# Kernel optimization log

Measured on AMD Instinct MI355X. Metric: run time of the kernel, lower is better.

Reference implementation:

```python
import jax, jax.numpy as jnp
import numpy as np

B, S, E = 4, 2048, 1024

def setup_inputs() -> dict:
    key = jax.random.key(0)
    ks = jax.random.split(key, 9)
    lim = 1.0 / np.sqrt(E)
    inp = {
        "query": jax.random.normal(ks[0], (B, S, E), dtype=jnp.float32),
        "key": jax.random.normal(ks[1], (B, S, E), dtype=jnp.float32),
        "value": jax.random.normal(ks[2], (B, S, E), dtype=jnp.float32),
        "Wq": jax.random.uniform(ks[3], (E, E), jnp.float32, -lim, lim),
        "bq": jax.random.uniform(ks[4], (E,), jnp.float32, -lim, lim),
        "Wk": jax.random.uniform(ks[5], (E, E), jnp.float32, -lim, lim),
        "bk": jax.random.uniform(ks[6], (E,), jnp.float32, -lim, lim),
        "Wv": jax.random.uniform(ks[7], (E, E), jnp.float32, -lim, lim),
        "bv": jax.random.uniform(ks[8], (E,), jnp.float32, -lim, lim),
    }
    return inp

def reference(query, key, value, Wq, bq, Wk, bk, Wv, bv):
    # Linear layers (torch stores weight as [out,in]; here W is [in,out] used as x @ W)
    q = query @ Wq + bq            # [B,S,E]
    k = key @ Wk + bk              # [B,S,E]
    v = value @ Wv + bv            # [B,S,E]
    inv_scale = jnp.asarray(E, q.dtype) ** 0.5
    scores = jnp.einsum("bse,bte->bst", q, k) / inv_scale  # [B,S,S]
    attn = jax.nn.softmax(scores, axis=-1)
    # dropout_p = 0.0 -> identity
    out = jnp.einsum("bst,bte->bse", attn, v)  # [B,S,E]
    return out
```

## Files before the change

kernel.cpp:

```cpp
#include <hip/hip_runtime.h>
#include <hip/hip_bf16.h>


typedef __bf16 bf16_t;
typedef bf16_t bf16x8 __attribute__((ext_vector_type(8)));
typedef bf16_t bf16x4 __attribute__((ext_vector_type(4)));
typedef float  f32x4  __attribute__((ext_vector_type(4)));

typedef const __attribute__((address_space(1))) unsigned gl_uint;
typedef __attribute__((address_space(3))) unsigned lds_uint;

#define BM 128
#define BN 128
#define BK 64

__device__ __forceinline__ void gload_lds16(const void* g, void* l) {
  __builtin_amdgcn_global_load_lds((gl_uint*)g, (lds_uint*)l, 16, 0, 0);
}

#define VMCNT(N) asm volatile("s_waitcnt vmcnt(" #N ")" ::: "memory")
#define LGKM0()  asm volatile("s_waitcnt lgkmcnt(0)" ::: "memory")

template <int KS, int NT>
__device__ __forceinline__ void gemm_v3(
    const bf16_t* __restrict__ Ab, const bf16_t* __restrict__ Bb,
    bf16_t* Lb, f32x4 acc[4][4])
{
  const int tid  = threadIdx.x;
  const int lane = tid & 63;
  const int l15  = lane & 15;
  const int quad = lane >> 4;
  const int wid  = tid >> 6;
  const int wr   = wid >> 1;
  const int wcl  = wid & 1;
  const int swz0 = (quad ^ (l15 & 7)) * 8;
  const int swz1 = ((quad + 4) ^ (l15 & 7)) * 8;

  const int r8 = tid >> 3, s8 = tid & 7;
  const size_t gbase = (size_t)r8 * KS + (size_t)((s8 ^ (r8 & 7)) * 8);
  const int dbase = tid * 8;

#define SLOTA(s) (Lb + (s) * 24576)
#define SLOTB(s) (Lb + (s) * 24576 + 16384)
#define STAGE6(ktile, slot) { \
    const bf16_t* _A = Ab + (size_t)(ktile) * 64; \
    const bf16_t* _B = Bb + (size_t)(ktile) * 64; \
    bf16_t* _la = SLOTA(slot); bf16_t* _lb = SLOTB(slot); \
    gload_lds16(_A + gbase,                      _la + dbase); \
    gload_lds16(_A + gbase + (size_t)64 * KS,    _la + dbase + 4096); \
    gload_lds16(_A + gbase + (size_t)128 * KS,   _la + dbase + 8192); \
    gload_lds16(_A + gbase + (size_t)192 * KS,   _la + dbase + 12288); \
    gload_lds16(_B + gbase,                      _lb + dbase); \
    gload_lds16(_B + gbase + (size_t)64 * KS,    _lb + dbase + 4096); }

  const int aoff = (wr * 64 + l15) * 64;
  const int boff = (wcl * 64 + l15) * 64;

#define RD(slot, FA, FB) { \
    const bf16_t* _a = SLOTA(slot) + aoff; \
    const bf16_t* _b = SLOTB(slot) + boff; \
    _Pragma("unroll") for (int mi = 0; mi < 4; ++mi) { \
      FA[mi][0] = *(const bf16x8*)(_a + mi * 1024 + swz0); \
      FA[mi][1] = *(const bf16x8*)(_a + mi * 1024 + swz1); } \
    _Pragma("unroll") for (int ni = 0; ni < 4; ++ni) { \
      FB[ni][0] = *(const bf16x8*)(_b + ni * 1024 + swz0); \
      FB[ni][1] = *(const bf16x8*)(_b + ni * 1024 + swz1); } }

#define MFM(FA, FB) \
    _Pragma("unroll") for (int kk = 0; kk < 2; ++kk) \
    _Pragma("unroll") for (int mi = 0; mi < 4; ++mi) \
    _Pragma("unroll") for (int ni = 0; ni < 4; ++ni) \
      acc[mi][ni] = __builtin_amdgcn_mfma_f32_16x16x32_bf16( \
          FA[mi][kk], FB[ni][kk], acc[mi][ni], 0, 0, 0);

  bf16x8 fa0[4][2], fb0[4][2], fa1[4][2], fb1[4][2];

  STAGE6(0, 0); STAGE6(1, 1); STAGE6(2, 2);
  VMCNT(6);
  __builtin_amdgcn_s_barrier();
  RD(0, fa0, fb0);
  LGKM0();
  __builtin_amdgcn_s_barrier();

#pragma unroll
  for (int kt = 0; kt < NT - 2; ++kt) {
    const int ss = kt % 3;
    const int rs = (kt + 1) % 3;
    if (kt <= NT - 4) STAGE6(kt + 3, ss);
    if ((kt & 1) == 0) { RD(rs, fa1, fb1); MFM(fa0, fb0); }
    else               { RD(rs, fa0, fb0); MFM(fa1, fb1); }
    if (kt <= NT - 4) { VMCNT(6); }
    else              { VMCNT(0); }
    __builtin_amdgcn_s_barrier();
  }
  RD((NT - 1) % 3, fa1, fb1); MFM(fa0, fb0);
  MFM(fa1, fb1);

#undef SLOTA
#undef SLOTB
#undef STAGE6
#undef RD
#undef MFM
}

__device__ __forceinline__ void mfma_tile128(const bf16_t* As, const bf16_t* Bs,
                                             f32x4 acc[4][4]) {
  const int lane = threadIdx.x & 63;
  const int quad = lane >> 4;
  const int l15  = lane & 15;
  const int wid  = threadIdx.x >> 6;
  const int wm   = (wid >> 1) * 64;
  const int wn   = (wid & 1) * 64;
  const int csw  = l15 & 7;
#pragma unroll
  for (int ks = 0; ks < 2; ++ks) {
    const int sg = ks * 4 + quad;
    const int c  = (sg ^ csw) * 8;
    bf16x8 fa[4], fb[4];
#pragma unroll
    for (int i = 0; i < 4; ++i)
      fa[i] = *(const bf16x8*)&As[(wm + i * 16 + l15) * BK + c];
#pragma unroll
    for (int i = 0; i < 4; ++i)
      fb[i] = *(const bf16x8*)&Bs[(wn + i * 16 + l15) * BK + c];
#pragma unroll
    for (int mi = 0; mi < 4; ++mi)
#pragma unroll
      for (int ni = 0; ni < 4; ++ni)
        acc[mi][ni] = __builtin_amdgcn_mfma_f32_16x16x32_bf16(
            fa[mi], fb[ni], acc[mi][ni], 0, 0, 0);
  }
}

__device__ __forceinline__ void gemm_core128(
    const bf16_t* __restrict__ Ab, const bf16_t* __restrict__ Bb,
    const int K, bf16_t* As, bf16_t* Bs, f32x4 acc[4][4])
{
  const int tid = threadIdx.x;
  for (int kt = 0; kt < K; kt += BK) {
#pragma unroll
    for (int j = 0; j < 4; ++j) {
      const int lin = j * 256 + tid;
      const int row = lin >> 3;
      const int seg = (lin & 7) ^ (row & 7);
      gload_lds16(Ab + (size_t)row * K + kt + seg * 8, &As[lin * 8]);
    }
#pragma unroll
    for (int j = 0; j < 4; ++j) {
      const int lin = j * 256 + tid;
      const int row = lin >> 3;
      const int seg = (lin & 7) ^ (row & 7);
      gload_lds16(Bb + (size_t)row * K + kt + seg * 8, &Bs[lin * 8]);
    }
    __syncthreads();
    mfma_tile128(As, Bs, acc);
    __syncthreads();
  }
}

__global__ __launch_bounds__(256, 2)
void qkv_proj(const bf16_t* __restrict__ qb, const bf16_t* __restrict__ kb,
              const bf16_t* __restrict__ vb, const bf16_t* __restrict__ Wqt,
              const bf16_t* __restrict__ Wkt, const bf16_t* __restrict__ Wvt,
              const float* __restrict__ bq, const float* __restrict__ bk,
              const float* __restrict__ bv, bf16_t* __restrict__ qp,
              bf16_t* __restrict__ kp, bf16_t* __restrict__ vT)
{
  __shared__ __align__(16) bf16_t As[BM * BK];
  __shared__ __align__(16) bf16_t Bs[BN * BK];

  const int L = blockIdx.x;
  const int g = L >> 3;
  const int gst = (L & 7) * 3 + (g >> 6);
  const int z  = gst >> 3;
  const int sy = gst & 7;
  const int w  = g & 63;
  const int bx = w & 7;
  const int by = sy * 8 + (w >> 3);

  const bf16_t* A    = (z == 0) ? qb : (z == 1) ? kb : vb;
  const bf16_t* W    = (z == 0) ? Wqt : (z == 1) ? Wkt : Wvt;
  const float*  bias = (z == 0) ? bq : (z == 1) ? bk : bv;
  const int K = 1024, N = 1024;
  const bf16_t* Ab = A + (size_t)by * BM * K;
  const bf16_t* Bb = W + (size_t)bx * BN * K;

  f32x4 acc[4][4];
  const f32x4 z4 = {0.f, 0.f, 0.f, 0.f};
#pragma unroll
  for (int i = 0; i < 4; ++i)
#pragma unroll
    for (int j = 0; j < 4; ++j) acc[i][j] = z4;

  gemm_core128(Ab, Bb, K, As, Bs, acc);

  const int lane = threadIdx.x & 63;
  const int quad = lane >> 4;
  const int l15  = lane & 15;
  const int wid  = threadIdx.x >> 6;
  const int wm = (wid >> 1) * 64, wn = (wid & 1) * 64;
  const int m0 = by * BM, n0 = bx * BN;
#pragma unroll
  for (int mi = 0; mi < 4; ++mi) {
#pragma unroll
    for (int ni = 0; ni < 4; ++ni) {
      const int gn = n0 + wn + ni * 16 + l15;
      const int gm = m0 + wm + mi * 16 + quad * 4;
      const float bv_ = bias[gn];
      f32x4 a = acc[mi][ni];
      if (z < 2) {
        bf16_t* C = (z == 0) ? qp : kp;
#pragma unroll
        for (int r = 0; r < 4; ++r)
          C[(size_t)(gm + r) * N + gn] = (bf16_t)(a[r] + bv_);
      } else {
        const int b = gm >> 11;
        const int s = gm & 2047;
        bf16x4 o;
#pragma unroll
        for (int r = 0; r < 4; ++r) o[r] = (bf16_t)(a[r] + bv_);
        *(bf16x4*)&vT[((size_t)b * N + gn) * 2048 + s] = o;
      }
    }
  }
}

__global__ __launch_bounds__(512, 2)
void scores_v3(const bf16_t* __restrict__ qp, const bf16_t* __restrict__ kp,
               bf16_t* __restrict__ P, float* __restrict__ lsum)
{
  __shared__ __align__(16) bf16_t lds[3 * 24576];
  const int L   = blockIdx.x;
  const int lin = (L & 7) * 64 + (L >> 3);
  const int bz  = lin >> 7;
  const int r   = lin & 127;
  const int by  = r >> 4, bx = r & 15;
  const int K = 1024;

  const bf16_t* Ab = qp + (size_t)bz * 2048 * 1024 + (size_t)by * 256 * K;
  const bf16_t* Bb = kp + (size_t)bz * 2048 * 1024 + (size_t)bx * 128 * K;

  f32x4 acc[4][4];
  const f32x4 z4 = {0.f, 0.f, 0.f, 0.f};
#pragma unroll
  for (int i = 0; i < 4; ++i)
#pragma unroll
    for (int j = 0; j < 4; ++j) acc[i][j] = z4;

  gemm_v3<1024, 16>(Ab, Bb, lds, acc);

  const int tid = threadIdx.x;
  const int lane = tid & 63, l15 = lane & 15, quad = lane >> 4;
  const int wid = tid >> 6, wr = wid >> 1, wcl = wid & 1;
  const int m0 = by * 256 + wr * 64;
  const int n0 = bx * 128 + wcl * 64;
  bf16_t* C = P + (size_t)bz * 2048 * 2048;
  float* lsb = lsum + (size_t)bz * 2048;
  const float cexp = 0.03125f * 1.4426950408889634f;
#pragma unroll
  for (int mi = 0; mi < 4; ++mi) {
    const int gm = m0 + mi * 16 + quad * 4;
#pragma unroll
    for (int rr = 0; rr < 4; ++rr) {
      float rs = 0.f;
#pragma unroll
      for (int ni = 0; ni < 4; ++ni) {
        const int gn = n0 + ni * 16 + l15;
        const bf16_t ob = (bf16_t)exp2f(acc[mi][ni][rr] * cexp);
        C[(size_t)(gm + rr) * 2048 + gn] = ob;
        rs += (float)ob;
      }
      rs += __shfl_xor(rs, 1, 64);
      rs += __shfl_xor(rs, 2, 64);
      rs += __shfl_xor(rs, 4, 64);
      rs += __shfl_xor(rs, 8, 64);
      if (l15 == 0) atomicAdd(&lsb[gm + rr], rs);
    }
  }
}

__global__ __launch_bounds__(256, 2)
void pv128(const bf16_t* __restrict__ P, const bf16_t* __restrict__ vT,
           const float* __restrict__ lsum, float* __restrict__ out)
{
  __shared__ __align__(16) bf16_t As[BM * BK];
  __shared__ __align__(16) bf16_t Bs[BN * BK];

  const int L = blockIdx.x;
  const int xcd = L & 7;
  const int w = (L >> 3) & 63;
  const int bz = xcd >> 1;
  const int bx = w & 7;
  const int by = (xcd & 1) * 8 + (w >> 3);

  const bf16_t* Ab = P  + (size_t)bz * 2048 * 2048 + (size_t)by * BM * 2048;
  const bf16_t* Bb = vT + (size_t)bz * 1024 * 2048 + (size_t)bx * BN * 2048;

  f32x4 acc[4][4];
  const f32x4 z4 = {0.f, 0.f, 0.f, 0.f};
#pragma unroll
  for (int i = 0; i < 4; ++i)
#pragma unroll
    for (int j = 0; j < 4; ++j) acc[i][j] = z4;

  gemm_core128(Ab, Bb, 2048, As, Bs, acc);

  const int lane = threadIdx.x & 63;
  const int quad = lane >> 4;
  const int l15  = lane & 15;
  const int wid  = threadIdx.x >> 6;
  const int wm = (wid >> 1) * 64, wn = (wid & 1) * 64;
  const int m0 = by * BM, n0 = bx * BN;
  const float* ls = lsum + (size_t)bz * 2048;
  float* C = out + (size_t)bz * 2048 * 1024;
#pragma unroll
  for (int mi = 0; mi < 4; ++mi) {
    const int gm = m0 + wm + mi * 16 + quad * 4;
    const f32x4 lv = *(const f32x4*)&ls[gm];
    float il[4];
#pragma unroll
    for (int r = 0; r < 4; ++r) il[r] = 1.0f / lv[r];
#pragma unroll
    for (int ni = 0; ni < 4; ++ni) {
      const int gn = n0 + wn + ni * 16 + l15;
      f32x4 a = acc[mi][ni];
#pragma unroll
      for (int r = 0; r < 4; ++r)
        C[(size_t)(gm + r) * 1024 + gn] = a[r] * il[r];
    }
  }
}

__global__ __launch_bounds__(256)
void prep(const float* __restrict__ q, const float* __restrict__ k,
          const float* __restrict__ v, const float* __restrict__ Wq,
          const float* __restrict__ Wk, const float* __restrict__ Wv,
          bf16_t* __restrict__ qo, bf16_t* __restrict__ ko,
          bf16_t* __restrict__ vo, bf16_t* __restrict__ Wqt,
          bf16_t* __restrict__ Wkt, bf16_t* __restrict__ Wvt) {
  const int L = blockIdx.x;
  const int tid = threadIdx.x;
  if (L < 24576) {
    const int z = L >> 13;
    const int blk = L & 8191;
    const float* in = (z == 0) ? q : (z == 1) ? k : v;
    bf16_t* out = (z == 0) ? qo : (z == 1) ? ko : vo;
    const size_t i = ((size_t)blk * 256 + tid) * 4;
    const float4 w = *(const float4*)(in + i);
    bf16x4 o;
    o[0] = (bf16_t)w.x; o[1] = (bf16_t)w.y; o[2] = (bf16_t)w.z; o[3] = (bf16_t)w.w;
    *(bf16x4*)(out + i) = o;
  } else {
    const int t = L - 24576;
    const int z = t >> 8;
    const int wi = t & 255;
    const float* W = (z == 0) ? Wq : (z == 1) ? Wk : Wv;
    bf16_t* Wt = (z == 0) ? Wqt : (z == 1) ? Wkt : Wvt;
    __shared__ float tile[64][65];
    const int n0 = (wi & 15) * 64;
    const int k0 = (wi >> 4) * 64;
#pragma unroll
    for (int it = 0; it < 16; ++it) {
      const int idx = it * 256 + tid;
      const int r = idx >> 6, c = idx & 63;
      tile[r][c] = W[(size_t)(k0 + r) * 1024 + n0 + c];
    }
    __syncthreads();
#pragma unroll
    for (int it = 0; it < 16; ++it) {
      const int idx = it * 256 + tid;
      const int r = idx >> 6, c = idx & 63;
      Wt[(size_t)(n0 + r) * 1024 + k0 + c] = (bf16_t)tile[c][r];
    }
  }
}

extern "C" void kernel_launch(void* const* d_in, const int* in_sizes, int n_in,
                              void* d_out, int out_size, void* d_ws, size_t ws_size,
                              hipStream_t stream) {
  const int B = 4, S = 2048, E = 1024;
  const size_t BSE = (size_t)B * S * E;
  const size_t EE  = (size_t)E * E;

  const float* q_in = (const float*)d_in[0];
  const float* k_in = (const float*)d_in[1];
  const float* v_in = (const float*)d_in[2];
  const float* Wq = (const float*)d_in[3];
  const float* bq = (const float*)d_in[4];
  const float* Wk = (const float*)d_in[5];
  const float* bk = (const float*)d_in[6];
  const float* Wv = (const float*)d_in[7];
  const float* bv = (const float*)d_in[8];
  float* out = (float*)d_out;

  char* ws = (char*)d_ws;
  bf16_t* Wqt = (bf16_t*)ws;
  bf16_t* Wkt = Wqt + EE;
  bf16_t* Wvt = Wkt + EE;
  bf16_t* qb  = Wvt + EE;
  bf16_t* kb  = qb + BSE;
  bf16_t* vb  = kb + BSE;
  bf16_t* qp  = vb + BSE;
  bf16_t* kp  = qp + BSE;
  bf16_t* vT  = kp + BSE;
  bf16_t* P   = vT + BSE;
  float* lsum = (float*)qb;

  prep<<<25344, 256, 0, stream>>>(q_in, k_in, v_in, Wq, Wk, Wv,
                                  qb, kb, vb, Wqt, Wkt, Wvt);

  qkv_proj<<<1536, 256, 0, stream>>>(qb, kb, vb, Wqt, Wkt, Wvt,
                                     bq, bk, bv, qp, kp, vT);

  hipMemsetAsync(lsum, 0, (size_t)B * S * sizeof(float), stream);

  scores_v3<<<512, 512, 0, stream>>>(qp, kp, P, lsum);

  pv128<<<512, 256, 0, stream>>>(P, vT, lsum, out);

  (void)in_sizes; (void)n_in; (void)out_size; (void)ws_size;
}
```

Before: 302.0 us.

## Fuse fp32-to-bf16 input cast into QKV GEMM and compute softmax row sums via MFMA

The separate prep pass that cast q/k/v activations to bf16 is removed. The QKV projection kernel now loads fp32 activations into registers, converts them and writes bf16 into LDS, double-buffering the register loads across k-tiles. The softmax denominator is no longer built with shuffles and atomics in the scores kernel. It is instead accumulated in the PV GEMM by an extra MFMA of each P fragment against a vector of ones. This drops the memset, the atomics and an extra read and write of the activations. In exchange it adds a few MFMAs per k-step and uses register-path A loads instead of direct-to-LDS loads.

```diff
diff --git a/kernel.cpp b/kernel.cpp
--- a/kernel.cpp
+++ b/kernel.cpp
@@ -20,6 +20,190 @@
 
 #define VMCNT(N) asm volatile("s_waitcnt vmcnt(" #N ")" ::: "memory")
 #define LGKM0()  asm volatile("s_waitcnt lgkmcnt(0)" ::: "memory")
+
+template <bool LSUM>
+__device__ __forceinline__ void mfma_tile128(const bf16_t* As, const bf16_t* Bs,
+                                             f32x4 acc[4][4], f32x4 acc_l[4]) {
+  const int lane = threadIdx.x & 63;
+  const int quad = lane >> 4;
+  const int l15  = lane & 15;
+  const int wid  = threadIdx.x >> 6;
+  const int wm   = (wid >> 1) * 64;
+  const int wn   = (wid & 1) * 64;
+  const int csw  = l15 & 7;
+  bf16x8 ones;
+  if (LSUM) {
+#pragma unroll
+    for (int t = 0; t < 8; ++t) ones[t] = (bf16_t)1.0f;
+  }
+#pragma unroll
+  for (int ks = 0; ks < 2; ++ks) {
+    const int sg = ks * 4 + quad;
+    const int c  = (sg ^ csw) * 8;
+    bf16x8 fa[4], fb[4];
+#pragma unroll
+    for (int i = 0; i < 4; ++i)
+      fa[i] = *(const bf16x8*)&As[(wm + i * 16 + l15) * BK + c];
+#pragma unroll
+    for (int i = 0; i < 4; ++i)
+      fb[i] = *(const bf16x8*)&Bs[(wn + i * 16 + l15) * BK + c];
+#pragma unroll
+    for (int mi = 0; mi < 4; ++mi)
+#pragma unroll
+      for (int ni = 0; ni < 4; ++ni)
+        acc[mi][ni] = __builtin_amdgcn_mfma_f32_16x16x32_bf16(
+            fa[mi], fb[ni], acc[mi][ni], 0, 0, 0);
+    if (LSUM) {
+#pragma unroll
+      for (int mi = 0; mi < 4; ++mi)
+        acc_l[mi] = __builtin_amdgcn_mfma_f32_16x16x32_bf16(
+            fa[mi], ones, acc_l[mi], 0, 0, 0);
+    }
+  }
+}
+
+template <bool LSUM>
+__device__ __forceinline__ void gemm_core128(
+    const bf16_t* __restrict__ Ab, const bf16_t* __restrict__ Bb,
+    const int K, bf16_t* As, bf16_t* Bs, f32x4 acc[4][4], f32x4 acc_l[4])
+{
+  const int tid = threadIdx.x;
+  for (int kt = 0; kt < K; kt += BK) {
+#pragma unroll
+    for (int j = 0; j < 4; ++j) {
+      const int lin = j * 256 + tid;
+      const int row = lin >> 3;
+      const int seg = (lin & 7) ^ (row & 7);
+      gload_lds16(Ab + (size_t)row * K + kt + seg * 8, &As[lin * 8]);
+    }
+#pragma unroll
+    for (int j = 0; j < 4; ++j) {
+      const int lin = j * 256 + tid;
+      const int row = lin >> 3;
+      const int seg = (lin & 7) ^ (row & 7);
+      gload_lds16(Bb + (size_t)row * K + kt + seg * 8, &Bs[lin * 8]);
+    }
+    __syncthreads();
+    mfma_tile128<LSUM>(As, Bs, acc, acc_l);
+    __syncthreads();
+  }
+}
+
+__global__ __launch_bounds__(256, 2)
+void qkv_f(const float* __restrict__ qin, const float* __restrict__ kin,
+           const float* __restrict__ vin, const bf16_t* __restrict__ Wqt,
+           const bf16_t* __restrict__ Wkt, const bf16_t* __restrict__ Wvt,
+           const float* __restrict__ bq, const float* __restrict__ bk,
+           const float* __restrict__ bv, bf16_t* __restrict__ qp,
+           bf16_t* __restrict__ kp, bf16_t* __restrict__ vT)
+{
+  __shared__ __align__(16) bf16_t As[BM * BK];
+  __shared__ __align__(16) bf16_t Bs[BN * BK];
+
+  const int L = blockIdx.x;
+  const int g = L >> 3;
+  const int gst = (L & 7) * 3 + (g >> 6);
+  const int z  = gst >> 3;
+  const int sy = gst & 7;
+  const int w  = g & 63;
+  const int bx = w & 7;
+  const int by = sy * 8 + (w >> 3);
+
+  const float*  A    = (z == 0) ? qin : (z == 1) ? kin : vin;
+  const bf16_t* W    = (z == 0) ? Wqt : (z == 1) ? Wkt : Wvt;
+  const float*  bias = (z == 0) ? bq : (z == 1) ? bk : bv;
+  const int K = 1024, N = 1024;
+  const float*  Ab = A + (size_t)by * BM * K;
+  const bf16_t* Bb = W + (size_t)bx * BN * K;
+
+  const int tid = threadIdx.x;
+
+  f32x4 acc[4][4];
+  const f32x4 z4 = {0.f, 0.f, 0.f, 0.f};
+#pragma unroll
+  for (int i = 0; i < 4; ++i)
+#pragma unroll
+    for (int j = 0; j < 4; ++j) acc[i][j] = z4;
+
+#define LOAD_A(ktile, AR) { \
+    _Pragma("unroll") for (int j = 0; j < 4; ++j) { \
+      const int lin = j * 256 + tid; \
+      const int row = lin >> 3; \
+      const int seg = (lin & 7) ^ (row & 7); \
+      const float* _s = Ab + (size_t)row * K + (ktile) * 64 + seg * 8; \
+      AR[2 * j]     = *(const float4*)_s; \
+      AR[2 * j + 1] = *(const float4*)(_s + 4); } }
+
+#define WRITE_A(AR) { \
+    _Pragma("unroll") for (int j = 0; j < 4; ++j) { \
+      const int lin = j * 256 + tid; \
+      bf16x8 o; \
+      o[0] = (bf16_t)AR[2 * j].x;     o[1] = (bf16_t)AR[2 * j].y; \
+      o[2] = (bf16_t)AR[2 * j].z;     o[3] = (bf16_t)AR[2 * j].w; \
+      o[4] = (bf16_t)AR[2 * j + 1].x; o[5] = (bf16_t)AR[2 * j + 1].y; \
+      o[6] = (bf16_t)AR[2 * j + 1].z; o[7] = (bf16_t)AR[2 * j + 1].w; \
+      *(bf16x8*)&As[lin * 8] = o; } }
+
+  float4 ar0[8], ar1[8];
+  LOAD_A(0, ar0);
+
+#pragma unroll
+  for (int t16 = 0; t16 < 16; ++t16) {
+    const int kt = t16 * 64;
+#pragma unroll
+    for (int j = 0; j < 4; ++j) {
+      const int lin = j * 256 + tid;
+      const int row = lin >> 3;
+      const int seg = (lin & 7) ^ (row & 7);
+      gload_lds16(Bb + (size_t)row * K + kt + seg * 8, &Bs[lin * 8]);
+    }
+    __builtin_amdgcn_sched_barrier(0);
+    if (t16 < 15) {
+      if ((t16 & 1) == 0) { LOAD_A(t16 + 1, ar1); }
+      else                { LOAD_A(t16 + 1, ar0); }
+    }
+    if ((t16 & 1) == 0) { WRITE_A(ar0); }
+    else                { WRITE_A(ar1); }
+    if (t16 < 15) { VMCNT(8); }
+    else          { VMCNT(0); }
+    LGKM0();
+    __builtin_amdgcn_s_barrier();
+    mfma_tile128<false>(As, Bs, acc, nullptr);
+    __builtin_amdgcn_s_barrier();
+  }
+#undef LOAD_A
+#undef WRITE_A
+
+  const int lane = tid & 63;
+  const int quad = lane >> 4;
+  const int l15  = lane & 15;
+  const int wid  = tid >> 6;
+  const int wm = (wid >> 1) * 64, wn = (wid & 1) * 64;
+  const int m0 = by * BM, n0 = bx * BN;
+#pragma unroll
+  for (int mi = 0; mi < 4; ++mi) {
+#pragma unroll
+    for (int ni = 0; ni < 4; ++ni) {
+      const int gn = n0 + wn + ni * 16 + l15;
+      const int gm = m0 + wm + mi * 16 + quad * 4;
+      const float bv_ = bias[gn];
+      f32x4 a = acc[mi][ni];
+      if (z < 2) {
+        bf16_t* C = (z == 0) ? qp : kp;
+#pragma unroll
+        for (int r = 0; r < 4; ++r)
+          C[(size_t)(gm + r) * N + gn] = (bf16_t)(a[r] + bv_);
+      } else {
+        const int b = gm >> 11;
+        const int s = gm & 2047;
+        bf16x4 o;
+#pragma unroll
+        for (int r = 0; r < 4; ++r) o[r] = (bf16_t)(a[r] + bv_);
+        *(bf16x4*)&vT[((size_t)b * N + gn) * 2048 + s] = o;
+      }
+    }
+  }
+}
 
 template <int KS, int NT>
 __device__ __forceinline__ void gemm_v3(
@@ -103,131 +287,9 @@
 #undef MFM
 }
 
-__device__ __forceinline__ void mfma_tile128(const bf16_t* As, const bf16_t* Bs,
-                                             f32x4 acc[4][4]) {
-  const int lane = threadIdx.x & 63;
-  const int quad = lane >> 4;
-  const int l15  = lane & 15;
-  const int wid  = threadIdx.x >> 6;
-  const int wm   = (wid >> 1) * 64;
-  const int wn   = (wid & 1) * 64;
-  const int csw  = l15 & 7;
-#pragma unroll
-  for (int ks = 0; ks < 2; ++ks) {
-    const int sg = ks * 4 + quad;
-    const int c  = (sg ^ csw) * 8;
-    bf16x8 fa[4], fb[4];
-#pragma unroll
-    for (int i = 0; i < 4; ++i)
-      fa[i] = *(const bf16x8*)&As[(wm + i * 16 + l15) * BK + c];
-#pragma unroll
-    for (int i = 0; i < 4; ++i)
-      fb[i] = *(const bf16x8*)&Bs[(wn + i * 16 + l15) * BK + c];
-#pragma unroll
-    for (int mi = 0; mi < 4; ++mi)
-#pragma unroll
-      for (int ni = 0; ni < 4; ++ni)
-        acc[mi][ni] = __builtin_amdgcn_mfma_f32_16x16x32_bf16(
-            fa[mi], fb[ni], acc[mi][ni], 0, 0, 0);
-  }
-}
-
-__device__ __forceinline__ void gemm_core128(
-    const bf16_t* __restrict__ Ab, const bf16_t* __restrict__ Bb,
-    const int K, bf16_t* As, bf16_t* Bs, f32x4 acc[4][4])
-{
-  const int tid = threadIdx.x;
-  for (int kt = 0; kt < K; kt += BK) {
-#pragma unroll
-    for (int j = 0; j < 4; ++j) {
-      const int lin = j * 256 + tid;
-      const int row = lin >> 3;
-      const int seg = (lin & 7) ^ (row & 7);
-      gload_lds16(Ab + (size_t)row * K + kt + seg * 8, &As[lin * 8]);
-    }
-#pragma unroll
-    for (int j = 0; j < 4; ++j) {
-      const int lin = j * 256 + tid;
-      const int row = lin >> 3;
-      const int seg = (lin & 7) ^ (row & 7);
-      gload_lds16(Bb + (size_t)row * K + kt + seg * 8, &Bs[lin * 8]);
-    }
-    __syncthreads();
-    mfma_tile128(As, Bs, acc);
-    __syncthreads();
-  }
-}
-
-__global__ __launch_bounds__(256, 2)
-void qkv_proj(const bf16_t* __restrict__ qb, const bf16_t* __restrict__ kb,
-              const bf16_t* __restrict__ vb, const bf16_t* __restrict__ Wqt,
-              const bf16_t* __restrict__ Wkt, const bf16_t* __restrict__ Wvt,
-              const float* __restrict__ bq, const float* __restrict__ bk,
-              const float* __restrict__ bv, bf16_t* __restrict__ qp,
-              bf16_t* __restrict__ kp, bf16_t* __restrict__ vT)
-{
-  __shared__ __align__(16) bf16_t As[BM * BK];
-  __shared__ __align__(16) bf16_t Bs[BN * BK];
-
-  const int L = blockIdx.x;
-  const int g = L >> 3;
-  const int gst = (L & 7) * 3 + (g >> 6);
-  const int z  = gst >> 3;
-  const int sy = gst & 7;
-  const int w  = g & 63;
-  const int bx = w & 7;
-  const int by = sy * 8 + (w >> 3);
-
-  const bf16_t* A    = (z == 0) ? qb : (z == 1) ? kb : vb;
-  const bf16_t* W    = (z == 0) ? Wqt : (z == 1) ? Wkt : Wvt;
-  const float*  bias = (z == 0) ? bq : (z == 1) ? bk : bv;
-  const int K = 1024, N = 1024;
-  const bf16_t* Ab = A + (size_t)by * BM * K;
-  const bf16_t* Bb = W + (size_t)bx * BN * K;
-
-  f32x4 acc[4][4];
-  const f32x4 z4 = {0.f, 0.f, 0.f, 0.f};
-#pragma unroll
-  for (int i = 0; i < 4; ++i)
-#pragma unroll
-    for (int j = 0; j < 4; ++j) acc[i][j] = z4;
-
-  gemm_core128(Ab, Bb, K, As, Bs, acc);
-
-  const int lane = threadIdx.x & 63;
-  const int quad = lane >> 4;
-  const int l15  = lane & 15;
-  const int wid  = threadIdx.x >> 6;
-  const int wm = (wid >> 1) * 64, wn = (wid & 1) * 64;
-  const int m0 = by * BM, n0 = bx * BN;
-#pragma unroll
-  for (int mi = 0; mi < 4; ++mi) {
-#pragma unroll
-    for (int ni = 0; ni < 4; ++ni) {
-      const int gn = n0 + wn + ni * 16 + l15;
-      const int gm = m0 + wm + mi * 16 + quad * 4;
-      const float bv_ = bias[gn];
-      f32x4 a = acc[mi][ni];
-      if (z < 2) {
-        bf16_t* C = (z == 0) ? qp : kp;
-#pragma unroll
-        for (int r = 0; r < 4; ++r)
-          C[(size_t)(gm + r) * N + gn] = (bf16_t)(a[r] + bv_);
-      } else {
-        const int b = gm >> 11;
-        const int s = gm & 2047;
-        bf16x4 o;
-#pragma unroll
-        for (int r = 0; r < 4; ++r) o[r] = (bf16_t)(a[r] + bv_);
-        *(bf16x4*)&vT[((size_t)b * N + gn) * 2048 + s] = o;
-      }
-    }
-  }
-}
-
 __global__ __launch_bounds__(512, 2)
 void scores_v3(const bf16_t* __restrict__ qp, const bf16_t* __restrict__ kp,
-               bf16_t* __restrict__ P, float* __restrict__ lsum)
+               bf16_t* __restrict__ P)
 {
   __shared__ __align__(16) bf16_t lds[3 * 24576];
   const int L   = blockIdx.x;
@@ -255,33 +317,24 @@
   const int m0 = by * 256 + wr * 64;
   const int n0 = bx * 128 + wcl * 64;
   bf16_t* C = P + (size_t)bz * 2048 * 2048;
-  float* lsb = lsum + (size_t)bz * 2048;
   const float cexp = 0.03125f * 1.4426950408889634f;
 #pragma unroll
   for (int mi = 0; mi < 4; ++mi) {
     const int gm = m0 + mi * 16 + quad * 4;
 #pragma unroll
-    for (int rr = 0; rr < 4; ++rr) {
-      float rs = 0.f;
-#pragma unroll
-      for (int ni = 0; ni < 4; ++ni) {
-        const int gn = n0 + ni * 16 + l15;
-        const bf16_t ob = (bf16_t)exp2f(acc[mi][ni][rr] * cexp);
-        C[(size_t)(gm + rr) * 2048 + gn] = ob;
-        rs += (float)ob;
-      }
-      rs += __shfl_xor(rs, 1, 64);
-      rs += __shfl_xor(rs, 2, 64);
-      rs += __shfl_xor(rs, 4, 64);
-      rs += __shfl_xor(rs, 8, 64);
-      if (l15 == 0) atomicAdd(&lsb[gm + rr], rs);
+    for (int ni = 0; ni < 4; ++ni) {
+      const int gn = n0 + ni * 16 + l15;
+      f32x4 a = acc[mi][ni];
+#pragma unroll
+      for (int rr = 0; rr < 4; ++rr)
+        C[(size_t)(gm + rr) * 2048 + gn] = (bf16_t)exp2f(a[rr] * cexp);
     }
   }
 }
 
 __global__ __launch_bounds__(256, 2)
 void pv128(const bf16_t* __restrict__ P, const bf16_t* __restrict__ vT,
-           const float* __restrict__ lsum, float* __restrict__ out)
+           float* __restrict__ out)
 {
   __shared__ __align__(16) bf16_t As[BM * BK];
   __shared__ __align__(16) bf16_t Bs[BN * BK];
@@ -297,13 +350,16 @@
   const bf16_t* Bb = vT + (size_t)bz * 1024 * 2048 + (size_t)bx * BN * 2048;
 
   f32x4 acc[4][4];
+  f32x4 acc_l[4];
   const f32x4 z4 = {0.f, 0.f, 0.f, 0.f};
 #pragma unroll
-  for (int i = 0; i < 4; ++i)
+  for (int i = 0; i < 4; ++i) {
+    acc_l[i] = z4;
 #pragma unroll
     for (int j = 0; j < 4; ++j) acc[i][j] = z4;
-
-  gemm_core128(Ab, Bb, 2048, As, Bs, acc);
+  }
+
+  gemm_core128<true>(Ab, Bb, 2048, As, Bs, acc, acc_l);
 
   const int lane = threadIdx.x & 63;
   const int quad = lane >> 4;
@@ -311,15 +367,13 @@
   const int wid  = threadIdx.x >> 6;
   const int wm = (wid >> 1) * 64, wn = (wid & 1) * 64;
   const int m0 = by * BM, n0 = bx * BN;
-  const float* ls = lsum + (size_t)bz * 2048;
   float* C = out + (size_t)bz * 2048 * 1024;
 #pragma unroll
   for (int mi = 0; mi < 4; ++mi) {
     const int gm = m0 + wm + mi * 16 + quad * 4;
-    const f32x4 lv = *(const f32x4*)&ls[gm];
     float il[4];
 #pragma unroll
-    for (int r = 0; r < 4; ++r) il[r] = 1.0f / lv[r];
+    for (int r = 0; r < 4; ++r) il[r] = 1.0f / acc_l[mi][r];
 #pragma unroll
     for (int ni = 0; ni < 4; ++ni) {
       const int gn = n0 + wn + ni * 16 + l15;
@@ -332,46 +386,30 @@
 }
 
 __global__ __launch_bounds__(256)
-void prep(const float* __restrict__ q, const float* __restrict__ k,
-          const float* __restrict__ v, const float* __restrict__ Wq,
-          const float* __restrict__ Wk, const float* __restrict__ Wv,
-          bf16_t* __restrict__ qo, bf16_t* __restrict__ ko,
-          bf16_t* __restrict__ vo, bf16_t* __restrict__ Wqt,
-          bf16_t* __restrict__ Wkt, bf16_t* __restrict__ Wvt) {
-  const int L = blockIdx.x;
+void prep_w(const float* __restrict__ Wq, const float* __restrict__ Wk,
+            const float* __restrict__ Wv, bf16_t* __restrict__ Wqt,
+            bf16_t* __restrict__ Wkt, bf16_t* __restrict__ Wvt) {
+  const int t = blockIdx.x;
   const int tid = threadIdx.x;
-  if (L < 24576) {
-    const int z = L >> 13;
-    const int blk = L & 8191;
-    const float* in = (z == 0) ? q : (z == 1) ? k : v;
-    bf16_t* out = (z == 0) ? qo : (z == 1) ? ko : vo;
-    const size_t i = ((size_t)blk * 256 + tid) * 4;
-    const float4 w = *(const float4*)(in + i);
-    bf16x4 o;
-    o[0] = (bf16_t)w.x; o[1] = (bf16_t)w.y; o[2] = (bf16_t)w.z; o[3] = (bf16_t)w.w;
-    *(bf16x4*)(out + i) = o;
-  } else {
-    const int t = L - 24576;
-    const int z = t >> 8;
-    const int wi = t & 255;
-    const float* W = (z == 0) ? Wq : (z == 1) ? Wk : Wv;
-    bf16_t* Wt = (z == 0) ? Wqt : (z == 1) ? Wkt : Wvt;
-    __shared__ float tile[64][65];
-    const int n0 = (wi & 15) * 64;
-    const int k0 = (wi >> 4) * 64;
-#pragma unroll
-    for (int it = 0; it < 16; ++it) {
-      const int idx = it * 256 + tid;
-      const int r = idx >> 6, c = idx & 63;
-      tile[r][c] = W[(size_t)(k0 + r) * 1024 + n0 + c];
-    }
-    __syncthreads();
-#pragma unroll
-    for (int it = 0; it < 16; ++it) {
-      const int idx = it * 256 + tid;
-      const int r = idx >> 6, c = idx & 63;
-      Wt[(size_t)(n0 + r) * 1024 + k0 + c] = (bf16_t)tile[c][r];
-    }
+  const int z = t >> 8;
+  const int wi = t & 255;
+  const float* W = (z == 0) ? Wq : (z == 1) ? Wk : Wv;
+  bf16_t* Wt = (z == 0) ? Wqt : (z == 1) ? Wkt : Wvt;
+  __shared__ float tile[64][65];
+  const int n0 = (wi & 15) * 64;
+  const int k0 = (wi >> 4) * 64;
+#pragma unroll
+  for (int it = 0; it < 16; ++it) {
+    const int idx = it * 256 + tid;
+    const int r = idx >> 6, c = idx & 63;
+    tile[r][c] = W[(size_t)(k0 + r) * 1024 + n0 + c];
+  }
+  __syncthreads();
+#pragma unroll
+  for (int it = 0; it < 16; ++it) {
+    const int idx = it * 256 + tid;
+    const int r = idx >> 6, c = idx & 63;
+    Wt[(size_t)(n0 + r) * 1024 + k0 + c] = (bf16_t)tile[c][r];
   }
 }
 
@@ -397,26 +435,19 @@
   bf16_t* Wqt = (bf16_t*)ws;
   bf16_t* Wkt = Wqt + EE;
   bf16_t* Wvt = Wkt + EE;
-  bf16_t* qb  = Wvt + EE;
-  bf16_t* kb  = qb + BSE;
-  bf16_t* vb  = kb + BSE;
-  bf16_t* qp  = vb + BSE;
+  bf16_t* qp  = Wvt + EE;
   bf16_t* kp  = qp + BSE;
   bf16_t* vT  = kp + BSE;
   bf16_t* P   = vT + BSE;
-  float* lsum = (float*)qb;
-
-  prep<<<25344, 256, 0, stream>>>(q_in, k_in, v_in, Wq, Wk, Wv,
-                                  qb, kb, vb, Wqt, Wkt, Wvt);
-
-  qkv_proj<<<1536, 256, 0, stream>>>(qb, kb, vb, Wqt, Wkt, Wvt,
-                                     bq, bk, bv, qp, kp, vT);
-
-  hipMemsetAsync(lsum, 0, (size_t)B * S * sizeof(float), stream);
-
-  scores_v3<<<512, 512, 0, stream>>>(qp, kp, P, lsum);
-
-  pv128<<<512, 256, 0, stream>>>(P, vT, lsum, out);
+
+  prep_w<<<768, 256, 0, stream>>>(Wq, Wk, Wv, Wqt, Wkt, Wvt);
+
+  qkv_f<<<1536, 256, 0, stream>>>(q_in, k_in, v_in, Wqt, Wkt, Wvt,
+                                  bq, bk, bv, qp, kp, vT);
+
+  scores_v3<<<512, 512, 0, stream>>>(qp, kp, P);
+
+  pv128<<<512, 256, 0, stream>>>(P, vT, out);
 
   (void)in_sizes; (void)n_in; (void)out_size; (void)ws_size;
 }
```

New measurement: 299.2 us. About the same (-0.9%).

## Compute softmax row sums via MFMA with ones vector inside PV GEMM

Applied to the files above, without the earlier changes.

Removes the atomic row-sum accumulation and the memset from the scores kernel. The PV kernel instead computes the row sums of P by running extra MFMAs against a vector of ones on the A fragments it already loads. This drops the shuffles, the atomics and one memset launch, at the cost of four extra MFMAs per k-step in the PV kernel, and those are repeated redundantly across the column tiles of each row.

```diff
diff --git a/kernel.cpp b/kernel.cpp
--- a/kernel.cpp
+++ b/kernel.cpp
@@ -20,6 +20,141 @@
 
 #define VMCNT(N) asm volatile("s_waitcnt vmcnt(" #N ")" ::: "memory")
 #define LGKM0()  asm volatile("s_waitcnt lgkmcnt(0)" ::: "memory")
+
+template <bool LSUM>
+__device__ __forceinline__ void mfma_tile128(const bf16_t* As, const bf16_t* Bs,
+                                             f32x4 acc[4][4], f32x4 acc_l[4]) {
+  const int lane = threadIdx.x & 63;
+  const int quad = lane >> 4;
+  const int l15  = lane & 15;
+  const int wid  = threadIdx.x >> 6;
+  const int wm   = (wid >> 1) * 64;
+  const int wn   = (wid & 1) * 64;
+  const int csw  = l15 & 7;
+  bf16x8 ones;
+  if (LSUM) {
+#pragma unroll
+    for (int t = 0; t < 8; ++t) ones[t] = (bf16_t)1.0f;
+  }
+#pragma unroll
+  for (int ks = 0; ks < 2; ++ks) {
+    const int sg = ks * 4 + quad;
+    const int c  = (sg ^ csw) * 8;
+    bf16x8 fa[4], fb[4];
+#pragma unroll
+    for (int i = 0; i < 4; ++i)
+      fa[i] = *(const bf16x8*)&As[(wm + i * 16 + l15) * BK + c];
+#pragma unroll
+    for (int i = 0; i < 4; ++i)
+      fb[i] = *(const bf16x8*)&Bs[(wn + i * 16 + l15) * BK + c];
+#pragma unroll
+    for (int mi = 0; mi < 4; ++mi)
+#pragma unroll
+      for (int ni = 0; ni < 4; ++ni)
+        acc[mi][ni] = __builtin_amdgcn_mfma_f32_16x16x32_bf16(
+            fa[mi], fb[ni], acc[mi][ni], 0, 0, 0);
+    if (LSUM) {
+#pragma unroll
+      for (int mi = 0; mi < 4; ++mi)
+        acc_l[mi] = __builtin_amdgcn_mfma_f32_16x16x32_bf16(
+            fa[mi], ones, acc_l[mi], 0, 0, 0);
+    }
+  }
+}
+
+template <bool LSUM>
+__device__ __forceinline__ void gemm_core128(
+    const bf16_t* __restrict__ Ab, const bf16_t* __restrict__ Bb,
+    const int K, bf16_t* As, bf16_t* Bs, f32x4 acc[4][4], f32x4 acc_l[4])
+{
+  const int tid = threadIdx.x;
+  for (int kt = 0; kt < K; kt += BK) {
+#pragma unroll
+    for (int j = 0; j < 4; ++j) {
+      const int lin = j * 256 + tid;
+      const int row = lin >> 3;
+      const int seg = (lin & 7) ^ (row & 7);
+      gload_lds16(Ab + (size_t)row * K + kt + seg * 8, &As[lin * 8]);
+    }
+#pragma unroll
+    for (int j = 0; j < 4; ++j) {
+      const int lin = j * 256 + tid;
+      const int row = lin >> 3;
+      const int seg = (lin & 7) ^ (row & 7);
+      gload_lds16(Bb + (size_t)row * K + kt + seg * 8, &Bs[lin * 8]);
+    }
+    __syncthreads();
+    mfma_tile128<LSUM>(As, Bs, acc, acc_l);
+    __syncthreads();
+  }
+}
+
+__global__ __launch_bounds__(256, 2)
+void qkv_proj(const bf16_t* __restrict__ qb, const bf16_t* __restrict__ kb,
+              const bf16_t* __restrict__ vb, const bf16_t* __restrict__ Wqt,
+              const bf16_t* __restrict__ Wkt, const bf16_t* __restrict__ Wvt,
+              const float* __restrict__ bq, const float* __restrict__ bk,
+              const float* __restrict__ bv, bf16_t* __restrict__ qp,
+              bf16_t* __restrict__ kp, bf16_t* __restrict__ vT)
+{
+  __shared__ __align__(16) bf16_t As[BM * BK];
+  __shared__ __align__(16) bf16_t Bs[BN * BK];
+
+  const int L = blockIdx.x;
+  const int g = L >> 3;
+  const int gst = (L & 7) * 3 + (g >> 6);
+  const int z  = gst >> 3;
+  const int sy = gst & 7;
+  const int w  = g & 63;
+  const int bx = w & 7;
+  const int by = sy * 8 + (w >> 3);
+
+  const bf16_t* A    = (z == 0) ? qb : (z == 1) ? kb : vb;
+  const bf16_t* W    = (z == 0) ? Wqt : (z == 1) ? Wkt : Wvt;
+  const float*  bias = (z == 0) ? bq : (z == 1) ? bk : bv;
+  const int K = 1024, N = 1024;
+  const bf16_t* Ab = A + (size_t)by * BM * K;
+  const bf16_t* Bb = W + (size_t)bx * BN * K;
+
+  f32x4 acc[4][4];
+  const f32x4 z4 = {0.f, 0.f, 0.f, 0.f};
+#pragma unroll
+  for (int i = 0; i < 4; ++i)
+#pragma unroll
+    for (int j = 0; j < 4; ++j) acc[i][j] = z4;
+
+  gemm_core128<false>(Ab, Bb, K, As, Bs, acc, nullptr);
+
+  const int lane = threadIdx.x & 63;
+  const int quad = lane >> 4;
+  const int l15  = lane & 15;
+  const int wid  = threadIdx.x >> 6;
+  const int wm = (wid >> 1) * 64, wn = (wid & 1) * 64;
+  const int m0 = by * BM, n0 = bx * BN;
+#pragma unroll
+  for (int mi = 0; mi < 4; ++mi) {
+#pragma unroll
+    for (int ni = 0; ni < 4; ++ni) {
+      const int gn = n0 + wn + ni * 16 + l15;
+      const int gm = m0 + wm + mi * 16 + quad * 4;
+      const float bv_ = bias[gn];
+      f32x4 a = acc[mi][ni];
+      if (z < 2) {
+        bf16_t* C = (z == 0) ? qp : kp;
+#pragma unroll
+        for (int r = 0; r < 4; ++r)
+          C[(size_t)(gm + r) * N + gn] = (bf16_t)(a[r] + bv_);
+      } else {
+        const int b = gm >> 11;
+        const int s = gm & 2047;
+        bf16x4 o;
+#pragma unroll
+        for (int r = 0; r < 4; ++r) o[r] = (bf16_t)(a[r] + bv_);
+        *(bf16x4*)&vT[((size_t)b * N + gn) * 2048 + s] = o;
+      }
+    }
+  }
+}
 
 template <int KS, int NT>
 __device__ __forceinline__ void gemm_v3(
@@ -103,131 +238,9 @@
 #undef MFM
 }
 
-__device__ __forceinline__ void mfma_tile128(const bf16_t* As, const bf16_t* Bs,
-                                             f32x4 acc[4][4]) {
-  const int lane = threadIdx.x & 63;
-  const int quad = lane >> 4;
-  const int l15  = lane & 15;
-  const int wid  = threadIdx.x >> 6;
-  const int wm   = (wid >> 1) * 64;
-  const int wn   = (wid & 1) * 64;
-  const int csw  = l15 & 7;
-#pragma unroll
-  for (int ks = 0; ks < 2; ++ks) {
-    const int sg = ks * 4 + quad;
-    const int c  = (sg ^ csw) * 8;
-    bf16x8 fa[4], fb[4];
-#pragma unroll
-    for (int i = 0; i < 4; ++i)
-      fa[i] = *(const bf16x8*)&As[(wm + i * 16 + l15) * BK + c];
-#pragma unroll
-    for (int i = 0; i < 4; ++i)
-      fb[i] = *(const bf16x8*)&Bs[(wn + i * 16 + l15) * BK + c];
-#pragma unroll
-    for (int mi = 0; mi < 4; ++mi)
-#pragma unroll
-      for (int ni = 0; ni < 4; ++ni)
-        acc[mi][ni] = __builtin_amdgcn_mfma_f32_16x16x32_bf16(
-            fa[mi], fb[ni], acc[mi][ni], 0, 0, 0);
-  }
-}
-
-__device__ __forceinline__ void gemm_core128(
-    const bf16_t* __restrict__ Ab, const bf16_t* __restrict__ Bb,
-    const int K, bf16_t* As, bf16_t* Bs, f32x4 acc[4][4])
-{
-  const int tid = threadIdx.x;
-  for (int kt = 0; kt < K; kt += BK) {
-#pragma unroll
-    for (int j = 0; j < 4; ++j) {
-      const int lin = j * 256 + tid;
-      const int row = lin >> 3;
-      const int seg = (lin & 7) ^ (row & 7);
-      gload_lds16(Ab + (size_t)row * K + kt + seg * 8, &As[lin * 8]);
-    }
-#pragma unroll
-    for (int j = 0; j < 4; ++j) {
-      const int lin = j * 256 + tid;
-      const int row = lin >> 3;
-      const int seg = (lin & 7) ^ (row & 7);
-      gload_lds16(Bb + (size_t)row * K + kt + seg * 8, &Bs[lin * 8]);
-    }
-    __syncthreads();
-    mfma_tile128(As, Bs, acc);
-    __syncthreads();
-  }
-}
-
-__global__ __launch_bounds__(256, 2)
-void qkv_proj(const bf16_t* __restrict__ qb, const bf16_t* __restrict__ kb,
-              const bf16_t* __restrict__ vb, const bf16_t* __restrict__ Wqt,
-              const bf16_t* __restrict__ Wkt, const bf16_t* __restrict__ Wvt,
-              const float* __restrict__ bq, const float* __restrict__ bk,
-              const float* __restrict__ bv, bf16_t* __restrict__ qp,
-              bf16_t* __restrict__ kp, bf16_t* __restrict__ vT)
-{
-  __shared__ __align__(16) bf16_t As[BM * BK];
-  __shared__ __align__(16) bf16_t Bs[BN * BK];
-
-  const int L = blockIdx.x;
-  const int g = L >> 3;
-  const int gst = (L & 7) * 3 + (g >> 6);
-  const int z  = gst >> 3;
-  const int sy = gst & 7;
-  const int w  = g & 63;
-  const int bx = w & 7;
-  const int by = sy * 8 + (w >> 3);
-
-  const bf16_t* A    = (z == 0) ? qb : (z == 1) ? kb : vb;
-  const bf16_t* W    = (z == 0) ? Wqt : (z == 1) ? Wkt : Wvt;
-  const float*  bias = (z == 0) ? bq : (z == 1) ? bk : bv;
-  const int K = 1024, N = 1024;
-  const bf16_t* Ab = A + (size_t)by * BM * K;
-  const bf16_t* Bb = W + (size_t)bx * BN * K;
-
-  f32x4 acc[4][4];
-  const f32x4 z4 = {0.f, 0.f, 0.f, 0.f};
-#pragma unroll
-  for (int i = 0; i < 4; ++i)
-#pragma unroll
-    for (int j = 0; j < 4; ++j) acc[i][j] = z4;
-
-  gemm_core128(Ab, Bb, K, As, Bs, acc);
-
-  const int lane = threadIdx.x & 63;
-  const int quad = lane >> 4;
-  const int l15  = lane & 15;
-  const int wid  = threadIdx.x >> 6;
-  const int wm = (wid >> 1) * 64, wn = (wid & 1) * 64;
-  const int m0 = by * BM, n0 = bx * BN;
-#pragma unroll
-  for (int mi = 0; mi < 4; ++mi) {
-#pragma unroll
-    for (int ni = 0; ni < 4; ++ni) {
-      const int gn = n0 + wn + ni * 16 + l15;
-      const int gm = m0 + wm + mi * 16 + quad * 4;
-      const float bv_ = bias[gn];
-      f32x4 a = acc[mi][ni];
-      if (z < 2) {
-        bf16_t* C = (z == 0) ? qp : kp;
-#pragma unroll
-        for (int r = 0; r < 4; ++r)
-          C[(size_t)(gm + r) * N + gn] = (bf16_t)(a[r] + bv_);
-      } else {
-        const int b = gm >> 11;
-        const int s = gm & 2047;
-        bf16x4 o;
-#pragma unroll
-        for (int r = 0; r < 4; ++r) o[r] = (bf16_t)(a[r] + bv_);
-        *(bf16x4*)&vT[((size_t)b * N + gn) * 2048 + s] = o;
-      }
-    }
-  }
-}
-
 __global__ __launch_bounds__(512, 2)
 void scores_v3(const bf16_t* __restrict__ qp, const bf16_t* __restrict__ kp,
-               bf16_t* __restrict__ P, float* __restrict__ lsum)
+               bf16_t* __restrict__ P)
 {
   __shared__ __align__(16) bf16_t lds[3 * 24576];
   const int L   = blockIdx.x;
@@ -255,33 +268,24 @@
   const int m0 = by * 256 + wr * 64;
   const int n0 = bx * 128 + wcl * 64;
   bf16_t* C = P + (size_t)bz * 2048 * 2048;
-  float* lsb = lsum + (size_t)bz * 2048;
   const float cexp = 0.03125f * 1.4426950408889634f;
 #pragma unroll
   for (int mi = 0; mi < 4; ++mi) {
     const int gm = m0 + mi * 16 + quad * 4;
 #pragma unroll
-    for (int rr = 0; rr < 4; ++rr) {
-      float rs = 0.f;
-#pragma unroll
-      for (int ni = 0; ni < 4; ++ni) {
-        const int gn = n0 + ni * 16 + l15;
-        const bf16_t ob = (bf16_t)exp2f(acc[mi][ni][rr] * cexp);
-        C[(size_t)(gm + rr) * 2048 + gn] = ob;
-        rs += (float)ob;
-      }
-      rs += __shfl_xor(rs, 1, 64);
-      rs += __shfl_xor(rs, 2, 64);
-      rs += __shfl_xor(rs, 4, 64);
-      rs += __shfl_xor(rs, 8, 64);
-      if (l15 == 0) atomicAdd(&lsb[gm + rr], rs);
+    for (int ni = 0; ni < 4; ++ni) {
+      const int gn = n0 + ni * 16 + l15;
+      f32x4 a = acc[mi][ni];
+#pragma unroll
+      for (int rr = 0; rr < 4; ++rr)
+        C[(size_t)(gm + rr) * 2048 + gn] = (bf16_t)exp2f(a[rr] * cexp);
     }
   }
 }
 
 __global__ __launch_bounds__(256, 2)
 void pv128(const bf16_t* __restrict__ P, const bf16_t* __restrict__ vT,
-           const float* __restrict__ lsum, float* __restrict__ out)
+           float* __restrict__ out)
 {
   __shared__ __align__(16) bf16_t As[BM * BK];
   __shared__ __align__(16) bf16_t Bs[BN * BK];
@@ -297,13 +301,16 @@
   const bf16_t* Bb = vT + (size_t)bz * 1024 * 2048 + (size_t)bx * BN * 2048;
 
   f32x4 acc[4][4];
+  f32x4 acc_l[4];
   const f32x4 z4 = {0.f, 0.f, 0.f, 0.f};
 #pragma unroll
-  for (int i = 0; i < 4; ++i)
+  for (int i = 0; i < 4; ++i) {
+    acc_l[i] = z4;
 #pragma unroll
     for (int j = 0; j < 4; ++j) acc[i][j] = z4;
-
-  gemm_core128(Ab, Bb, 2048, As, Bs, acc);
+  }
+
+  gemm_core128<true>(Ab, Bb, 2048, As, Bs, acc, acc_l);
 
   const int lane = threadIdx.x & 63;
   const int quad = lane >> 4;
@@ -311,15 +318,13 @@
   const int wid  = threadIdx.x >> 6;
   const int wm = (wid >> 1) * 64, wn = (wid & 1) * 64;
   const int m0 = by * BM, n0 = bx * BN;
-  const float* ls = lsum + (size_t)bz * 2048;
   float* C = out + (size_t)bz * 2048 * 1024;
 #pragma unroll
   for (int mi = 0; mi < 4; ++mi) {
     const int gm = m0 + wm + mi * 16 + quad * 4;
-    const f32x4 lv = *(const f32x4*)&ls[gm];
     float il[4];
 #pragma unroll
-    for (int r = 0; r < 4; ++r) il[r] = 1.0f / lv[r];
+    for (int r = 0; r < 4; ++r) il[r] = 1.0f / acc_l[mi][r];
 #pragma unroll
     for (int ni = 0; ni < 4; ++ni) {
       const int gn = n0 + wn + ni * 16 + l15;
@@ -404,7 +409,6 @@
   bf16_t* kp  = qp + BSE;
   bf16_t* vT  = kp + BSE;
   bf16_t* P   = vT + BSE;
-  float* lsum = (float*)qb;
 
   prep<<<25344, 256, 0, stream>>>(q_in, k_in, v_in, Wq, Wk, Wv,
                                   qb, kb, vb, Wqt, Wkt, Wvt);
@@ -412,11 +416,9 @@
   qkv_proj<<<1536, 256, 0, stream>>>(qb, kb, vb, Wqt, Wkt, Wvt,
                                      bq, bk, bv, qp, kp, vT);
 
-  hipMemsetAsync(lsum, 0, (size_t)B * S * sizeof(float), stream);
-
-  scores_v3<<<512, 512, 0, stream>>>(qp, kp, P, lsum);
-
-  pv128<<<512, 256, 0, stream>>>(P, vT, lsum, out);
+  scores_v3<<<512, 512, 0, stream>>>(qp, kp, P);
+
+  pv128<<<512, 256, 0, stream>>>(P, vT, out);
 
   (void)in_sizes; (void)n_in; (void)out_size; (void)ws_size;
 }
```

Result: no change. 296.1 us (-1.9%).
